# Kernel optimization log

Measured on AMD Instinct MI355X. Metric: run time of the kernel, lower is better.

The kernel has to match this reference:

```python
import jax, jax.numpy as jnp
import numpy as np


def setup_inputs() -> dict:
    key = jax.random.key(0)
    k1, k2 = jax.random.split(key)
    B, T, C = 32, 512, 384
    MAX_LEN = 4096
    x = jax.random.normal(k1, (B, T, C), dtype=jnp.float32)
    duration = jax.random.randint(k2, (B, T), 0, 12, dtype=jnp.int64)
    return {"x": x, "duration": duration, "max_len": MAX_LEN}


def reference(x, duration, max_len):
    # x: [B, T, C] float; duration: [B, T] int; max_len: python int
    B, T, C = x.shape
    dur = jnp.maximum(duration, 0)            # original clamps expand_size at 0
    csum = jnp.cumsum(dur, axis=1)            # [B, T] exclusive boundaries (right edges)
    pos = jnp.arange(max_len)                 # [max_len]
    # source phoneme index for each output frame j: count of csum[b] <= j
    idx = jax.vmap(lambda c: jnp.searchsorted(c, pos, side="right"))(csum)  # [B, max_len]
    idx_c = jnp.clip(idx, 0, T - 1)
    out = jnp.take_along_axis(x, idx_c[:, :, None], axis=1)  # [B, max_len, C]
    mel_len = csum[:, -1]                     # [B] total expanded frames per batch
    valid = pos[None, :] < mel_len[:, None]   # [B, max_len], pad region -> 0
    out = out * valid[:, :, None].astype(out.dtype)
    return out, mel_len
```

## Files before the change

kernel.cpp:

```cpp
#include <hip/hip_runtime.h>
#include <hip/hip_bf16.h>


#define B   32
#define T   512
#define C4  96
#define ML  4096
#define PPB 128
#define TPB 384

typedef float v4f __attribute__((ext_vector_type(4)));

__global__ __launch_bounds__(TPB)
void lr_fused_kernel(const float* __restrict__ x,
                     const int* __restrict__ dur,
                     float* __restrict__ out,
                     float* __restrict__ mel_out) {
    __shared__ int s_cs[T];
    __shared__ int s_wsum[4];
    __shared__ int s_idx[PPB];

    const int b     = blockIdx.x >> 5;
    const int ptile = blockIdx.x & 31;
    const int tid   = threadIdx.x;
    const int lane  = tid & 63;

    int pairsum = 0, d1 = 0;
    if (tid < 256) {
        int2 d2 = ((const int2*)(dur + b * T))[tid];
        int d0 = d2.x < 0 ? 0 : d2.x;
        d1     = d2.y < 0 ? 0 : d2.y;
        pairsum = d0 + d1;
    }
    int incl = pairsum;
    #pragma unroll
    for (int off = 1; off < 64; off <<= 1) {
        int n = __shfl_up(incl, off, 64);
        if (lane >= off) incl += n;
    }
    if (tid < 256 && lane == 63) s_wsum[tid >> 6] = incl;
    __syncthreads();
    if (tid < 256) {
        const int w = tid >> 6;
        int wp = 0;
        #pragma unroll
        for (int j = 0; j < 3; ++j) if (j < w) wp += s_wsum[j];
        const int S = incl + wp;
        s_cs[2 * tid + 1] = S;
        s_cs[2 * tid]     = S - d1;
    }
    __syncthreads();

    const int mel = s_cs[T - 1];
    if (ptile == 0 && tid == 0) mel_out[b] = (float)mel;

    if (tid < PPB) {
        const int p = ptile * PPB + tid;
        int r = -1;
        if (p < mel) {
            int lo = 0, hi = T;
            while (lo < hi) {
                int mid = (lo + hi) >> 1;
                if (s_cs[mid] <= p) lo = mid + 1; else hi = mid;
            }
            r = lo < (T - 1) ? lo : (T - 1);
        }
        s_idx[tid] = r;
    }
    __syncthreads();

    const v4f* __restrict__ x4 = (const v4f*)x;
    v4f* __restrict__ o4 = (v4f*)out;
    const int sub = tid / 96;
    const int c4  = tid - sub * 96;
    const size_t xbase = (size_t)b * T * C4 + c4;
    const size_t obase = (size_t)b * ML * C4 + (size_t)ptile * PPB * C4 + c4;
    const v4f zero = (v4f){0.f, 0.f, 0.f, 0.f};

    #pragma unroll 8
    for (int k = 0; k < PPB / 4; ++k) {
        const int pl = 4 * k + sub;
        const int t  = s_idx[pl];
        v4f val = zero;
        if (t >= 0) val = x4[xbase + (size_t)t * C4];
        o4[obase + (size_t)pl * C4] = val;
    }
}

extern "C" void kernel_launch(void* const* d_in, const int* in_sizes, int n_in,
                              void* d_out, int out_size, void* d_ws, size_t ws_size,
                              hipStream_t stream) {
    const float* x   = (const float*)d_in[0];
    const int*   dur = (const int*)d_in[1];

    float* out     = (float*)d_out;
    float* mel_out = out + (size_t)B * ML * C4 * 4;

    const int grid = B * (ML / PPB);
    lr_fused_kernel<<<grid, TPB, 0, stream>>>(x, dur, out, mel_out);
}
```

Baseline: 227.2 us.

## Split into per-batch index setup kernel and lightweight gather-stream kernel

Moves the cumsum and searchsorted work into a separate per-batch setup kernel that writes int16 source indices to the workspace, using one binary search per 8 frames followed by a linear walk. The streaming kernel then only loads 64 indices and performs the gather-copy, with smaller tiles and more blocks. This removes the scan over the full duration row, which the fused kernel repeated in all 32 tiles of each batch. The cost is an extra kernel launch and a dependency between the two kernels. The old fused kernel is kept as a fallback for when the workspace is too small.

```diff
diff --git a/kernel.cpp b/kernel.cpp
--- a/kernel.cpp
+++ b/kernel.cpp
@@ -1,29 +1,26 @@
 #include <hip/hip_runtime.h>
-#include <hip/hip_bf16.h>
 
 
 #define B   32
 #define T   512
 #define C4  96
 #define ML  4096
-#define PPB 128
+#define PPB 64
 #define TPB 384
 
 typedef float v4f __attribute__((ext_vector_type(4)));
-
-__global__ __launch_bounds__(TPB)
-void lr_fused_kernel(const float* __restrict__ x,
-                     const int* __restrict__ dur,
-                     float* __restrict__ out,
+typedef unsigned short u16x8 __attribute__((ext_vector_type(8)));
+
+__global__ __launch_bounds__(512)
+void lr_setup_kernel(const int* __restrict__ dur,
+                     short* __restrict__ idx,
                      float* __restrict__ mel_out) {
     __shared__ int s_cs[T];
     __shared__ int s_wsum[4];
-    __shared__ int s_idx[PPB];
-
-    const int b     = blockIdx.x >> 5;
-    const int ptile = blockIdx.x & 31;
-    const int tid   = threadIdx.x;
-    const int lane  = tid & 63;
+
+    const int b    = blockIdx.x;
+    const int tid  = threadIdx.x;
+    const int lane = tid & 63;
 
     int pairsum = 0, d1 = 0;
     if (tid < 256) {
@@ -52,10 +49,106 @@
     __syncthreads();
 
     const int mel = s_cs[T - 1];
+    if (tid == 0) mel_out[b] = (float)mel;
+
+    const int p0 = tid * 8;
+    int lo = 0, hi = T;
+    while (lo < hi) {
+        int mid = (lo + hi) >> 1;
+        if (s_cs[mid] <= p0) lo = mid + 1; else hi = mid;
+    }
+    int t = lo;
+    u16x8 r;
+    #pragma unroll
+    for (int j = 0; j < 8; ++j) {
+        const int p = p0 + j;
+        if (p >= mel) {
+            r[j] = 0xFFFFu;
+        } else {
+            while (s_cs[t] <= p) ++t;
+            r[j] = (unsigned short)(t < (T - 1) ? t : (T - 1));
+        }
+    }
+    *((u16x8*)(idx + (size_t)b * ML) + tid) = r;
+}
+
+__global__ __launch_bounds__(TPB)
+void lr_stream_kernel(const float* __restrict__ x,
+                      const short* __restrict__ idx,
+                      float* __restrict__ out) {
+    __shared__ int s_idx[PPB];
+
+    const int b     = blockIdx.x >> 6;
+    const int ptile = blockIdx.x & 63;
+    const int tid   = threadIdx.x;
+
+    if (tid < PPB)
+        s_idx[tid] = (int)idx[(size_t)b * ML + ptile * PPB + tid];
+    __syncthreads();
+
+    const v4f* __restrict__ x4 = (const v4f*)x;
+    v4f* __restrict__ o4 = (v4f*)out;
+    const int sub = tid / 96;
+    const int c4  = tid - sub * 96;
+    const size_t xbase = (size_t)b * T * C4 + c4;
+    const size_t obase = (size_t)b * ML * C4 + (size_t)(ptile * PPB) * C4 + c4;
+    const v4f zero = (v4f){0.f, 0.f, 0.f, 0.f};
+
+    #pragma unroll 8
+    for (int k = 0; k < PPB / 4; ++k) {
+        const int pl = 4 * k + sub;
+        const int t  = s_idx[pl];
+        v4f val = zero;
+        if (t >= 0) val = x4[xbase + (size_t)t * C4];
+        o4[obase + (size_t)pl * C4] = val;
+    }
+}
+
+__global__ __launch_bounds__(384)
+void lr_fused_kernel(const float* __restrict__ x,
+                     const int* __restrict__ dur,
+                     float* __restrict__ out,
+                     float* __restrict__ mel_out) {
+    __shared__ int s_cs[T];
+    __shared__ int s_wsum[4];
+    __shared__ int s_idx[128];
+
+    const int b     = blockIdx.x >> 5;
+    const int ptile = blockIdx.x & 31;
+    const int tid   = threadIdx.x;
+    const int lane  = tid & 63;
+
+    int pairsum = 0, d1 = 0;
+    if (tid < 256) {
+        int2 d2 = ((const int2*)(dur + b * T))[tid];
+        int d0 = d2.x < 0 ? 0 : d2.x;
+        d1     = d2.y < 0 ? 0 : d2.y;
+        pairsum = d0 + d1;
+    }
+    int incl = pairsum;
+    #pragma unroll
+    for (int off = 1; off < 64; off <<= 1) {
+        int n = __shfl_up(incl, off, 64);
+        if (lane >= off) incl += n;
+    }
+    if (tid < 256 && lane == 63) s_wsum[tid >> 6] = incl;
+    __syncthreads();
+    if (tid < 256) {
+        const int w = tid >> 6;
+        int wp = 0;
+        #pragma unroll
+        for (int j = 0; j < 3; ++j) if (j < w) wp += s_wsum[j];
+        const int S = incl + wp;
+        s_cs[2 * tid + 1] = S;
+        s_cs[2 * tid]     = S - d1;
+    }
+    __syncthreads();
+
+    const int mel = s_cs[T - 1];
     if (ptile == 0 && tid == 0) mel_out[b] = (float)mel;
 
-    if (tid < PPB) {
-        const int p = ptile * PPB + tid;
+    if (tid < 128) {
+        const int p = ptile * 128 + tid;
         int r = -1;
         if (p < mel) {
             int lo = 0, hi = T;
@@ -74,11 +167,11 @@
     const int sub = tid / 96;
     const int c4  = tid - sub * 96;
     const size_t xbase = (size_t)b * T * C4 + c4;
-    const size_t obase = (size_t)b * ML * C4 + (size_t)ptile * PPB * C4 + c4;
+    const size_t obase = (size_t)b * ML * C4 + (size_t)ptile * 128 * C4 + c4;
     const v4f zero = (v4f){0.f, 0.f, 0.f, 0.f};
 
     #pragma unroll 8
-    for (int k = 0; k < PPB / 4; ++k) {
+    for (int k = 0; k < 128 / 4; ++k) {
         const int pl = 4 * k + sub;
         const int t  = s_idx[pl];
         v4f val = zero;
@@ -96,6 +189,12 @@
     float* out     = (float*)d_out;
     float* mel_out = out + (size_t)B * ML * C4 * 4;
 
-    const int grid = B * (ML / PPB);
-    lr_fused_kernel<<<grid, TPB, 0, stream>>>(x, dur, out, mel_out);
-}
+    const size_t idx_bytes = (size_t)B * ML * sizeof(short);
+    if (d_ws != nullptr && ws_size >= idx_bytes) {
+        short* idx = (short*)d_ws;
+        lr_setup_kernel<<<B, 512, 0, stream>>>(dur, idx, mel_out);
+        lr_stream_kernel<<<B * (ML / PPB), TPB, 0, stream>>>(x, idx, out);
+    } else {
+        lr_fused_kernel<<<B * (ML / 128), 384, 0, stream>>>(x, dur, out, mel_out);
+    }
+}
```

Measured after the change: 234.3 us. 3.1% more time.
